# Optimization experiments

Hardware: AMD Instinct MI355X
Metric: run time of the kernel (lower is better)

## Reference

```python
import jax, jax.numpy as jnp
import numpy as np

N_EMBD = 1024
N_HEAD = 16
HEAD_DIM = N_EMBD // N_HEAD
B, T = 4, 1024
EPS = 1e-5


def _linear_params(key, fan_in, fan_out):
    kw, kb = jax.random.split(key)
    bound = 1.0 / np.sqrt(fan_in)
    W = jax.random.uniform(kw, (fan_in, fan_out), minval=-bound, maxval=bound, dtype=jnp.float32)
    b = jax.random.uniform(kb, (fan_out,), minval=-bound, maxval=bound, dtype=jnp.float32)
    return W, b


def setup_inputs() -> dict:
    key = jax.random.key(0)
    ks = jax.random.split(key, 8)
    x = jax.random.normal(ks[0], (B, T, N_EMBD), dtype=jnp.float32)
    Wq, bq = _linear_params(ks[1], N_EMBD, N_EMBD)
    Wk, bk = _linear_params(ks[2], N_EMBD, N_EMBD)
    Wv, bv = _linear_params(ks[3], N_EMBD, N_EMBD)
    Wp, bp = _linear_params(ks[4], N_EMBD, N_EMBD)
    W1, b1 = _linear_params(ks[5], N_EMBD, 4 * N_EMBD)
    W2, b2 = _linear_params(ks[6], 4 * N_EMBD, N_EMBD)
    g1 = jnp.ones((N_EMBD,), jnp.float32); be1 = jnp.zeros((N_EMBD,), jnp.float32)
    g2 = jnp.ones((N_EMBD,), jnp.float32); be2 = jnp.zeros((N_EMBD,), jnp.float32)
    return {"x": x, "Wq": Wq, "bq": bq, "Wk": Wk, "bk": bk, "Wv": Wv, "bv": bv,
            "Wp": Wp, "bp": bp, "W1": W1, "b1": b1, "W2": W2, "b2": b2,
            "g1": g1, "be1": be1, "g2": g2, "be2": be2}


def _layernorm(x, g, b):
    mu = jnp.mean(x, axis=-1, keepdims=True)
    var = jnp.mean(jnp.square(x - mu), axis=-1, keepdims=True)
    return (x - mu) * jax.lax.rsqrt(var + EPS) * g + b


def _attention(x, Wq, bq, Wk, bk, Wv, bv, Wp, bp):
    Bsz, Tt, C = x.shape
    def heads(W, b):
        return (x @ W + b).reshape(Bsz, Tt, N_HEAD, HEAD_DIM).transpose(0, 2, 1, 3)  # [B,H,T,d]
    q, k, v = heads(Wq, bq), heads(Wk, bk), heads(Wv, bv)
    scores = jnp.einsum('bhqd,bhkd->bhqk', q, k) / np.sqrt(HEAD_DIM).astype(np.float32)
    causal = jnp.tril(jnp.ones((Tt, Tt), dtype=bool))
    scores = jnp.where(causal, scores, -jnp.inf)
    attn = jax.nn.softmax(scores, axis=-1)
    out = jnp.einsum('bhqk,bhkd->bhqd', attn, v)  # [B,H,T,d]
    out = out.transpose(0, 2, 1, 3).reshape(Bsz, Tt, C)
    return out @ Wp + bp


def _ff(x, W1, b1, W2, b2):
    h = jax.nn.gelu(x @ W1 + b1, approximate=False)  # torch nn.GELU default = exact erf
    return h @ W2 + b2


def reference(x, Wq, bq, Wk, bk, Wv, bv, Wp, bp, W1, b1, W2, b2, g1, be1, g2, be2):
    x = x + _attention(_layernorm(x, g1, be1), Wq, bq, Wk, bk, Wv, bv, Wp, bp)
    x = x + _ff(_layernorm(x, g2, be2), W1, b1, W2, b2)
    return x
```

## Files before the change

### kernel.cpp

```cpp
#include <hip/hip_runtime.h>
#include <hip/hip_bf16.h>

typedef __attribute__((ext_vector_type(8))) __bf16 bf16x8;
typedef __attribute__((ext_vector_type(4))) float f32x4;
typedef __attribute__((ext_vector_type(4))) unsigned short u16x4;
typedef unsigned short u16;

#define AS3(p) ((__attribute__((address_space(3))) void*)(p))
#define AS1(p) ((const __attribute__((address_space(1))) void*)(p))

#define QSCALE 0.18033688011112042f

__device__ __forceinline__ u16 f2b(float f) {
    __hip_bfloat16 h = __float2bfloat16(f);
    return __builtin_bit_cast(u16, h);
}

__device__ __forceinline__ float gelu_exact(float v) {
    const float z = v * 0.70710678118654752f;
    const float a = fabsf(z);
    const float t = __builtin_amdgcn_rcpf(1.0f + 0.3275911f * a);
    float p = 1.061405429f;
    p = p * t - 1.453152027f;
    p = p * t + 1.421413741f;
    p = p * t - 0.284496736f;
    p = p * t + 0.254829592f;
    p = p * t;
    float erfv = 1.0f - p * __expf(-a * a);
    erfv = copysignf(erfv, z);
    return 0.5f * v * (1.0f + erfv);
}

__global__ __launch_bounds__(256) void transpose_w(
    const float* __restrict__ W, u16* __restrict__ WT, int K, int N)
{
    __shared__ u16 tile[32][33];
    const int tx = threadIdx.x & 31, ty = threadIdx.x >> 5;
    const int n0 = blockIdx.x * 32, k0 = blockIdx.y * 32;
    #pragma unroll
    for (int p = 0; p < 4; ++p)
        tile[ty + p * 8][tx] = f2b(W[(size_t)(k0 + ty + p * 8) * N + n0 + tx]);
    __syncthreads();
    #pragma unroll
    for (int p = 0; p < 4; ++p)
        WT[(size_t)(n0 + ty + p * 8) * K + k0 + tx] = tile[tx][ty + p * 8];
}

__global__ __launch_bounds__(256) void transpose_w4(
    const float* __restrict__ W0, const float* __restrict__ W1,
    const float* __restrict__ W2, const float* __restrict__ W3,
    u16* __restrict__ WTqkv, u16* __restrict__ WTp)
{
    __shared__ u16 tile[32][33];
    const int z = blockIdx.z;
    const float* W = (z == 0) ? W0 : (z == 1) ? W1 : (z == 2) ? W2 : W3;
    u16* dst = (z == 3) ? WTp : WTqkv + (size_t)z * 1024 * 1024;
    const int tx = threadIdx.x & 31, ty = threadIdx.x >> 5;
    const int n0 = blockIdx.x * 32, k0 = blockIdx.y * 32;
    #pragma unroll
    for (int p = 0; p < 4; ++p)
        tile[ty + p * 8][tx] = f2b(W[(size_t)(k0 + ty + p * 8) * 1024 + n0 + tx]);
    __syncthreads();
    #pragma unroll
    for (int p = 0; p < 4; ++p)
        dst[(size_t)(n0 + ty + p * 8) * 1024 + k0 + tx] = tile[tx][ty + p * 8];
}

__global__ __launch_bounds__(256) void ln_bf16(
    const float* __restrict__ xin, const float* __restrict__ gam,
    const float* __restrict__ bet, u16* __restrict__ yout)
{
    __shared__ float red[8];
    const int row = blockIdx.x, tid = threadIdx.x;
    float4 v = ((const float4*)(xin + (size_t)row * 1024))[tid];
    float s = v.x + v.y + v.z + v.w;
    #pragma unroll
    for (int o = 32; o > 0; o >>= 1) s += __shfl_xor(s, o, 64);
    if ((tid & 63) == 0) red[tid >> 6] = s;
    __syncthreads();
    const float mu = (red[0] + red[1] + red[2] + red[3]) * (1.f / 1024.f);
    const float dx = v.x - mu, dy = v.y - mu, dz = v.z - mu, dw = v.w - mu;
    float sq = dx * dx + dy * dy + dz * dz + dw * dw;
    #pragma unroll
    for (int o = 32; o > 0; o >>= 1) sq += __shfl_xor(sq, o, 64);
    if ((tid & 63) == 0) red[4 + (tid >> 6)] = sq;
    __syncthreads();
    const float var = (red[4] + red[5] + red[6] + red[7]) * (1.f / 1024.f);
    const float inv = rsqrtf(var + 1e-5f);
    const float4 G = ((const float4*)gam)[tid];
    const float4 Bt = ((const float4*)bet)[tid];
    u16x4 o;
    o[0] = f2b(dx * inv * G.x + Bt.x);
    o[1] = f2b(dy * inv * G.y + Bt.y);
    o[2] = f2b(dz * inv * G.z + Bt.z);
    o[3] = f2b(dw * inv * G.w + Bt.w);
    ((u16x4*)(yout + (size_t)row * 1024))[tid] = o;
}

template <int MODE, int BM, int BN, int BK>
__global__ __launch_bounds__(256, 2) void gemm_bf16(
    const u16* __restrict__ A, const u16* __restrict__ BT,
    const float* __restrict__ b0, const float* __restrict__ b1,
    const float* __restrict__ b2,
    void* __restrict__ outp, int M, int N, int K)
{
    constexpr int WM = BM / 2;
    constexpr int MI = WM / 16;
    constexpr int NI = BN / 32;
    constexpr int KS = BK / 32;
    constexpr int AJ = BM * BK / 2048;
    constexpr int BJ = BN * BK / 2048;
    constexpr int LPS = AJ + BJ;
    constexpr int AELEM = BM * BK;
    constexpr int BELEM = BN * BK;
    constexpr int SLOTS = BK / 8;
    constexpr int RSH = (BK == 64) ? 3 : 2;
    constexpr int RPI = 64 >> RSH;
    __shared__ u16 Asm[3 * AELEM];
    __shared__ u16 Bsm[3 * BELEM];

    const int tid = threadIdx.x;
    const int lane = tid & 63, wid = tid >> 6;
    const int wm = wid >> 1, wn = wid & 1;
    const int g = lane >> 4, l16 = lane & 15;
    const int rkey = (BK == 64) ? (l16 & 7) : ((l16 >> 1) & 3);
    const int srow = lane >> RSH;
    const int sslot = (BK == 64) ? ((lane & 7) ^ (srow & 7))
                                 : ((lane & 3) ^ ((srow >> 1) & 3));

    const int nBN = N / BN;
    const int cpx = gridDim.x >> 3;
    const int wg = (blockIdx.x & 7) * cpx + (blockIdx.x >> 3);
    const int bm0 = (wg / nBN) * BM, bn0 = (wg % nBN) * BN;

    f32x4 acc[MI][NI] = {};

    const u16* aBase = A + (size_t)(bm0 + srow) * K + sslot * 8;
    const u16* bBase = BT + (size_t)(bn0 + srow) * K + sslot * 8;

    auto stage = [&](int kt, int buf) {
        u16* adst = Asm + buf * AELEM + lane * 8;
        u16* bdst = Bsm + buf * BELEM + lane * 8;
        #pragma unroll
        for (int j = 0; j < AJ; ++j) {
            const int ia = wid * AJ + j;
            __builtin_amdgcn_global_load_lds(AS1(aBase + (size_t)(ia * RPI) * K + kt),
                                             AS3(adst + ia * 512), 16, 0, 0);
        }
        #pragma unroll
        for (int j = 0; j < BJ; ++j) {
            const int ib = wid * BJ + j;
            __builtin_amdgcn_global_load_lds(AS1(bBase + (size_t)(ib * RPI) * K + kt),
                                             AS3(bdst + ib * 512), 16, 0, 0);
        }
    };

    const int nt = K / BK;
    stage(0, 0);
    stage(BK, 1);
    int cur = 0, pre = 2;

    for (int t = 0; t < nt; ++t) {
        if (t + 1 < nt) {
            if constexpr (LPS == 6)      asm volatile("s_waitcnt vmcnt(6)" ::: "memory");
            else if constexpr (LPS == 4) asm volatile("s_waitcnt vmcnt(4)" ::: "memory");
            else                         asm volatile("s_waitcnt vmcnt(3)" ::: "memory");
        } else {
            asm volatile("s_waitcnt vmcnt(0)" ::: "memory");
        }
        __builtin_amdgcn_s_barrier();
        __builtin_amdgcn_sched_barrier(0);

        const u16* asrc = Asm + cur * AELEM;
        const u16* bsrc = Bsm + cur * BELEM;
        bf16x8 af[KS][MI], bfr[KS][NI];
        #pragma unroll
        for (int ks = 0; ks < KS; ++ks) {
            #pragma unroll
            for (int mi = 0; mi < MI; ++mi) {
                const int r = wm * WM + mi * 16 + l16;
                const int slot = (ks * 4 + g) ^ rkey;
                af[ks][mi] = *(const bf16x8*)(asrc + r * BK + slot * 8);
            }
            #pragma unroll
            for (int ni = 0; ni < NI; ++ni) {
                const int c = wn * (BN / 2) + ni * 16 + l16;
                const int slot = (ks * 4 + g) ^ rkey;
                bfr[ks][ni] = *(const bf16x8*)(bsrc + c * BK + slot * 8);
            }
        }
        if (t + 2 < nt) stage((t + 2) * BK, pre);

        #pragma unroll
        for (int ks = 0; ks < KS; ++ks)
            #pragma unroll
            for (int mi = 0; mi < MI; ++mi)
                #pragma unroll
                for (int ni = 0; ni < NI; ++ni)
                    acc[mi][ni] = __builtin_amdgcn_mfma_f32_16x16x32_bf16(
                        af[ks][mi], bfr[ks][ni], acc[mi][ni], 0, 0, 0);

        pre = cur;
        cur = (cur == 2) ? 0 : cur + 1;
    }

    #pragma unroll
    for (int mi = 0; mi < MI; ++mi) {
        #pragma unroll
        for (int ni = 0; ni < NI; ++ni) {
            #pragma unroll
            for (int j = 0; j < 4; ++j) {
                const int m = bm0 + wm * WM + mi * 16 + g * 4 + j;
                const int n = bn0 + wn * (BN / 2) + ni * 16 + l16;
                float v = acc[mi][ni][j];
                if constexpr (MODE == 0) {
                    const float bias = (n < 1024) ? b0[n]
                                      : (n < 2048) ? b1[n - 1024] : b2[n - 2048];
                    float o = v + bias;
                    if (n < 1024) o *= QSCALE;
                    ((u16*)outp)[(size_t)m * N + n] = f2b(o);
                } else if constexpr (MODE == 1) {
                    ((float*)outp)[(size_t)m * N + n] =
                        v + b0[n] + b1[(size_t)m * N + n];
                } else {
                    ((u16*)outp)[(size_t)m * N + n] = f2b(gelu_exact(v + b0[n]));
                }
            }
        }
    }
}

__global__ __launch_bounds__(256) void attn_fwd(
    const u16* __restrict__ qkv, u16* __restrict__ outp)
{
    __shared__ u16 Ksm[2][64 * 64];
    __shared__ u16 Vsm[2][64 * 64];
    __shared__ u16 Psm[4][16 * 64];
    const int tid = threadIdx.x, lane = tid & 63, w = tid >> 6;
    const int lin = blockIdx.y * 8 + blockIdx.x;
    const int xq = (lin >> 3) & 7;
    const int bh = (((lin >> 6) & 7) << 3) | (lin & 7);
    const int b = bh >> 4, h = bh & 15;
    const int g = lane >> 4, l16 = lane & 15;
    const int skv = tid >> 4;
    const int sd4 = (tid & 15) * 4;

    const u16* kvb = qkv + (size_t)(b * 1024) * 3072 + 1024 + h * 64;

    bf16x8 vones;
    #pragma unroll
    for (int e = 0; e < 8; ++e) vones[e] = __builtin_bit_cast(__bf16, (u16)0x3F80);

    u16x4 kreg[4], vreg[4];
    auto issue = [&](int kv0) {
        const u16* kb = kvb + (size_t)kv0 * 3072;
        #pragma unroll
        for (int i = 0; i < 4; ++i)
            kreg[i] = *(const u16x4*)(kb + (size_t)(skv + 16 * i) * 3072 + sd4);
        #pragma unroll
        for (int i = 0; i < 4; ++i)
            vreg[i] = *(const u16x4*)(kb + (size_t)(4 * skv + i) * 3072 + 1024 + sd4);
    };
    auto stage_lds = [&](int buf) {
        #pragma unroll
        for (int i = 0; i < 4; ++i) {
            const int row = skv + 16 * i;
            *(u16x4*)(&Ksm[buf][row * 64 + (sd4 ^ ((row & 7) << 3))]) = kreg[i];
        }
        #pragma unroll
        for (int j = 0; j < 4; ++j) {
            u16x4 t;
            t[0] = vreg[0][j]; t[1] = vreg[1][j];
            t[2] = vreg[2][j]; t[3] = vreg[3][j];
            const int row = sd4 + j;
            *(u16x4*)(&Vsm[buf][row * 64 + ((4 * skv) ^ ((row & 7) << 3))]) = t;
        }
    };

    #pragma unroll
    for (int half = 0; half < 2; ++half) {
        const int qt = half ? (15 - xq) : xq;
        const int q0 = qt * 64;

        bf16x8 qf0, qf1;
        {
            const u16* qp = qkv + (size_t)(b * 1024 + q0 + w * 16 + l16) * 3072
                            + h * 64 + g * 8;
            qf0 = *(const bf16x8*)qp;
            qf1 = *(const bf16x8*)(qp + 32);
        }
        float m_run[4] = {-1e30f, -1e30f, -1e30f, -1e30f};
        float l_run[4] = {0.f, 0.f, 0.f, 0.f};
        f32x4 oacc[4] = {};

        issue(0);
        __syncthreads();
        stage_lds(0);
        if (qt > 0) issue(64);
        __syncthreads();
        int cur = 0;

        for (int kvt = 0; kvt <= qt; ++kvt) {
            f32x4 s[4];
            __builtin_amdgcn_s_setprio(1);
            #pragma unroll
            for (int t = 0; t < 4; ++t) {
                const int r = t * 16 + l16;
                const int sw = (r & 7) << 3;
                const bf16x8 kf0 = *(const bf16x8*)(&Ksm[cur][r * 64 + ((g * 8) ^ sw)]);
                const bf16x8 kf1 = *(const bf16x8*)(&Ksm[cur][r * 64 + (((g + 4) * 8) ^ sw)]);
                f32x4 z = {};
                z = __builtin_amdgcn_mfma_f32_16x16x32_bf16(qf0, kf0, z, 0, 0, 0);
                z = __builtin_amdgcn_mfma_f32_16x16x32_bf16(qf1, kf1, z, 0, 0, 0);
                s[t] = z;
            }
            __builtin_amdgcn_s_setprio(0);
            if (kvt == qt) {
                #pragma unroll
                for (int t = 0; t < 4; ++t)
                    #pragma unroll
                    for (int j = 0; j < 4; ++j) {
                        const int qrow = q0 + w * 16 + g * 4 + j;
                        const int kvc = q0 + t * 16 + l16;
                        if (kvc > qrow) s[t][j] = -1e30f;
                    }
            }
            float mx[4] = {-1e30f, -1e30f, -1e30f, -1e30f};
            #pragma unroll
            for (int t = 0; t < 4; ++t)
                #pragma unroll
                for (int j = 0; j < 4; ++j)
                    mx[j] = fmaxf(mx[j], s[t][j]);
            #pragma unroll
            for (int o = 1; o < 16; o <<= 1)
                #pragma unroll
                for (int j = 0; j < 4; ++j)
                    mx[j] = fmaxf(mx[j], __shfl_xor(mx[j], o, 16));
            float alpha[4];
            #pragma unroll
            for (int j = 0; j < 4; ++j) {
                const float mn = fmaxf(m_run[j], mx[j]);
                alpha[j] = __builtin_amdgcn_exp2f(m_run[j] - mn);
                m_run[j] = mn;
            }
            #pragma unroll
            for (int t = 0; t < 4; ++t)
                #pragma unroll
                for (int j = 0; j < 4; ++j)
                    s[t][j] = __builtin_amdgcn_exp2f(s[t][j] - m_run[j]);
            #pragma unroll
            for (int t = 0; t < 4; ++t)
                #pragma unroll
                for (int j = 0; j < 4; ++j) {
                    const int row = g * 4 + j;
                    Psm[w][row * 64 + ((t * 16 + l16) ^ ((row & 7) << 3))] = f2b(s[t][j]);
                }
            const int psw = (l16 & 7) << 3;
            const bf16x8 pf0 = *(const bf16x8*)(&Psm[w][l16 * 64 + ((g * 8) ^ psw)]);
            const bf16x8 pf1 = *(const bf16x8*)(&Psm[w][l16 * 64 + (((g + 4) * 8) ^ psw)]);
            f32x4 sum = {};
            sum = __builtin_amdgcn_mfma_f32_16x16x32_bf16(pf0, vones, sum, 0, 0, 0);
            sum = __builtin_amdgcn_mfma_f32_16x16x32_bf16(pf1, vones, sum, 0, 0, 0);
            #pragma unroll
            for (int j = 0; j < 4; ++j)
                l_run[j] = l_run[j] * alpha[j] + sum[j];
            #pragma unroll
            for (int dt = 0; dt < 4; ++dt)
                #pragma unroll
                for (int j = 0; j < 4; ++j)
                    oacc[dt][j] *= alpha[j];
            __builtin_amdgcn_s_setprio(1);
            #pragma unroll
            for (int dt = 0; dt < 4; ++dt) {
                const int rv = dt * 16 + l16;
                const int sw = (rv & 7) << 3;
                const bf16x8 vf0 = *(const bf16x8*)(&Vsm[cur][rv * 64 + ((g * 8) ^ sw)]);
                const bf16x8 vf1 = *(const bf16x8*)(&Vsm[cur][rv * 64 + (((g + 4) * 8) ^ sw)]);
                oacc[dt] = __builtin_amdgcn_mfma_f32_16x16x32_bf16(pf0, vf0, oacc[dt], 0, 0, 0);
                oacc[dt] = __builtin_amdgcn_mfma_f32_16x16x32_bf16(pf1, vf1, oacc[dt], 0, 0, 0);
            }
            __builtin_amdgcn_s_setprio(0);
            if (kvt < qt) {
                stage_lds(cur ^ 1);
                if (kvt + 2 <= qt) issue((kvt + 2) * 64);
                __syncthreads();
                cur ^= 1;
            }
        }
        #pragma unroll
        for (int j = 0; j < 4; ++j) l_run[j] = __builtin_amdgcn_rcpf(l_run[j]);
        #pragma unroll
        for (int dt = 0; dt < 4; ++dt)
            #pragma unroll
            for (int j = 0; j < 4; ++j) {
                const int m = b * 1024 + q0 + w * 16 + g * 4 + j;
                const int col = h * 64 + dt * 16 + l16;
                outp[(size_t)m * 1024 + col] = f2b(oacc[dt][j] * l_run[j]);
            }
    }
}

extern "C" void kernel_launch(void* const* d_in, const int* in_sizes, int n_in,
                              void* d_out, int out_size, void* d_ws, size_t ws_size,
                              hipStream_t stream)
{
    const float* x   = (const float*)d_in[0];
    const float* Wq  = (const float*)d_in[1];
    const float* bq  = (const float*)d_in[2];
    const float* Wk  = (const float*)d_in[3];
    const float* bk  = (const float*)d_in[4];
    const float* Wv  = (const float*)d_in[5];
    const float* bv  = (const float*)d_in[6];
    const float* Wp  = (const float*)d_in[7];
    const float* bp  = (const float*)d_in[8];
    const float* W1  = (const float*)d_in[9];
    const float* b1  = (const float*)d_in[10];
    const float* W2  = (const float*)d_in[11];
    const float* b2  = (const float*)d_in[12];
    const float* g1  = (const float*)d_in[13];
    const float* be1 = (const float*)d_in[14];
    const float* g2  = (const float*)d_in[15];
    const float* be2 = (const float*)d_in[16];

    char* ws = (char*)d_ws;
    const size_t MB = 1024 * 1024;
    u16*   ln_buf = (u16*)(ws);
    u16*   qkv    = (u16*)(ws + 8 * MB);
    u16*   attn_o = (u16*)(ws + 32 * MB);
    float* x1     = (float*)(ws + 40 * MB);
    u16*   hbuf   = (u16*)(ws + 56 * MB);
    u16*   wqkvT  = (u16*)(ws + 88 * MB);
    u16*   wpT    = (u16*)(ws + 94 * MB);
    u16*   w1T    = (u16*)(ws + 96 * MB);
    u16*   w2T    = (u16*)(ws + 104 * MB);

    transpose_w4<<<dim3(32, 32, 4), 256, 0, stream>>>(Wq, Wk, Wv, Wp, wqkvT, wpT);
    transpose_w<<<dim3(128, 32), 256, 0, stream>>>(W1, w1T, 1024, 4096);
    transpose_w<<<dim3(32, 128), 256, 0, stream>>>(W2, w2T, 4096, 1024);

    ln_bf16<<<4096, 256, 0, stream>>>(x, g1, be1, ln_buf);
    gemm_bf16<0, 128, 128, 32><<<768, 256, 0, stream>>>(
        ln_buf, wqkvT, bq, bk, bv, qkv, 4096, 3072, 1024);
    attn_fwd<<<dim3(8, 64), 256, 0, stream>>>(qkv, attn_o);
    gemm_bf16<1, 128, 64, 64><<<512, 256, 0, stream>>>(
        attn_o, wpT, bp, x, nullptr, x1, 4096, 1024, 1024);
    ln_bf16<<<4096, 256, 0, stream>>>(x1, g2, be2, ln_buf);
    gemm_bf16<2, 256, 128, 32><<<512, 256, 0, stream>>>(
        ln_buf, w1T, b1, nullptr, nullptr, hbuf, 4096, 4096, 1024);
    gemm_bf16<1, 128, 64, 64><<<512, 256, 0, stream>>>(
        hbuf, w2T, b2, x1, nullptr, (float*)d_out, 4096, 1024, 4096);
}
```

Before: 193.5 us.

## Add dedicated 256x256-tile, 512-thread FF1 GEMM with 4-stage LDS pipeline

```diff
diff --git a/kernel.cpp b/kernel.cpp
--- a/kernel.cpp
+++ b/kernel.cpp
@@ -113,7 +113,6 @@
     constexpr int LPS = AJ + BJ;
     constexpr int AELEM = BM * BK;
     constexpr int BELEM = BN * BK;
-    constexpr int SLOTS = BK / 8;
     constexpr int RSH = (BK == 64) ? 3 : 2;
     constexpr int RPI = 64 >> RSH;
     __shared__ u16 Asm[3 * AELEM];
@@ -228,6 +227,96 @@
             }
         }
     }
+}
+
+__global__ __launch_bounds__(512, 2) void gemm_ff1(
+    const u16* __restrict__ A, const u16* __restrict__ BT,
+    const float* __restrict__ b0, u16* __restrict__ outp)
+{
+    constexpr int AELEM = 256 * 32;
+    __shared__ u16 Asm[4 * AELEM];
+    __shared__ u16 Bsm[4 * AELEM];
+    const int K = 1024, N = 4096;
+
+    const int tid = threadIdx.x;
+    const int lane = tid & 63, wid = tid >> 6;
+    const int wr = wid >> 2, wc = wid & 3;
+    const int g = lane >> 4, l16 = lane & 15;
+    const int rkey = (l16 >> 1) & 3;
+    const int srow = lane >> 2;
+    const int sslot = (lane & 3) ^ ((srow >> 1) & 3);
+
+    const int wg = (blockIdx.x & 7) * 32 + (blockIdx.x >> 3);
+    const int bm0 = (wg >> 4) * 256, bn0 = (wg & 15) * 256;
+
+    f32x4 acc[8][4] = {};
+
+    const u16* aBase = A + (size_t)(bm0 + srow) * K + sslot * 8;
+    const u16* bBase = BT + (size_t)(bn0 + srow) * K + sslot * 8;
+
+    auto stage = [&](int kt, int buf) {
+        u16* adst = Asm + buf * AELEM + lane * 8;
+        u16* bdst = Bsm + buf * AELEM + lane * 8;
+        #pragma unroll
+        for (int j = 0; j < 2; ++j) {
+            const int ia = wid * 2 + j;
+            __builtin_amdgcn_global_load_lds(AS1(aBase + (size_t)(ia * 16) * K + kt),
+                                             AS3(adst + ia * 512), 16, 0, 0);
+        }
+        #pragma unroll
+        for (int j = 0; j < 2; ++j) {
+            const int ib = wid * 2 + j;
+            __builtin_amdgcn_global_load_lds(AS1(bBase + (size_t)(ib * 16) * K + kt),
+                                             AS3(bdst + ib * 512), 16, 0, 0);
+        }
+    };
+
+    const int nt = 32;
+    stage(0, 0); stage(32, 1); stage(64, 2);
+    int cur = 0;
+
+    for (int t = 0; t < nt; ++t) {
+        if (t + 2 < nt)      asm volatile("s_waitcnt vmcnt(8)" ::: "memory");
+        else if (t + 1 < nt) asm volatile("s_waitcnt vmcnt(4)" ::: "memory");
+        else                 asm volatile("s_waitcnt vmcnt(0)" ::: "memory");
+        __builtin_amdgcn_s_barrier();
+        __builtin_amdgcn_sched_barrier(0);
+
+        const u16* asrc = Asm + cur * AELEM;
+        const u16* bsrc = Bsm + cur * AELEM;
+        bf16x8 af[8], bfr[4];
+        #pragma unroll
+        for (int mi = 0; mi < 8; ++mi) {
+            const int r = wr * 128 + mi * 16 + l16;
+            af[mi] = *(const bf16x8*)(asrc + r * 32 + ((g ^ rkey) << 3));
+        }
+        #pragma unroll
+        for (int ni = 0; ni < 4; ++ni) {
+            const int c = wc * 64 + ni * 16 + l16;
+            bfr[ni] = *(const bf16x8*)(bsrc + c * 32 + ((g ^ rkey) << 3));
+        }
+        if (t + 3 < nt) stage((t + 3) * 32, (t + 3) & 3);
+
+        #pragma unroll
+        for (int mi = 0; mi < 8; ++mi)
+            #pragma unroll
+            for (int ni = 0; ni < 4; ++ni)
+                acc[mi][ni] = __builtin_amdgcn_mfma_f32_16x16x32_bf16(
+                    af[mi], bfr[ni], acc[mi][ni], 0, 0, 0);
+
+        cur = (cur + 1) & 3;
+    }
+
+    #pragma unroll
+    for (int mi = 0; mi < 8; ++mi)
+        #pragma unroll
+        for (int ni = 0; ni < 4; ++ni)
+            #pragma unroll
+            for (int j = 0; j < 4; ++j) {
+                const int m = bm0 + wr * 128 + mi * 16 + g * 4 + j;
+                const int n = bn0 + wc * 64 + ni * 16 + l16;
+                outp[(size_t)m * N + n] = f2b(gelu_exact(acc[mi][ni][j] + b0[n]));
+            }
 }
 
 __global__ __launch_bounds__(256) void attn_fwd(
@@ -445,8 +534,8 @@
     gemm_bf16<1, 128, 64, 64><<<512, 256, 0, stream>>>(
         attn_o, wpT, bp, x, nullptr, x1, 4096, 1024, 1024);
     ln_bf16<<<4096, 256, 0, stream>>>(x1, g2, be2, ln_buf);
-    gemm_bf16<2, 256, 128, 32><<<512, 256, 0, stream>>>(
-        ln_buf, w1T, b1, nullptr, nullptr, hbuf, 4096, 4096, 1024);
+    gemm_ff1<<<256, 512, 0, stream>>>(
+        ln_buf, w1T, b1, hbuf);
     gemm_bf16<1, 128, 64, 64><<<512, 256, 0, stream>>>(
         hbuf, w2T, b2, x1, nullptr, (float*)d_out, 4096, 1024, 4096);
 }
```

Result: faster. 189.0 us (-2.3%).
